# Performance work log

Measured on AMD Instinct MI355X. Metric: run time of the kernel, lower is better.

## Reference

```python
import jax, jax.numpy as jnp
import numpy as np

N = 100000      # nodes on each bipartite side
E = 1600000     # edges
D_IN = 128      # input feature dim
H, C = 2, 50    # heads, per-head out channels
B = 64          # graphs in batch
NEG_SLOPE = 0.2 # GATConv leaky_relu slope


def setup_inputs() -> dict:
    key = jax.random.key(0)
    ks = jax.random.split(key, 12)
    glorot = lambda k, shape: (jax.random.uniform(k, shape, jnp.float32, -1.0, 1.0)
                               * jnp.sqrt(6.0 / (shape[0] + shape[-1])))
    return {
        "x_s": jax.random.normal(ks[0], (N, D_IN), jnp.float32),
        "x_t": jax.random.normal(ks[1], (N, D_IN), jnp.float32),
        "edge_index": jax.random.randint(ks[2], (2, E), 0, N, jnp.int64),
        "distances": jax.random.uniform(ks[3], (E,), jnp.float32),
        "x_s_batch": jnp.sort(jax.random.randint(ks[4], (N,), 0, B, jnp.int64)),
        "x_t_batch": jnp.sort(jax.random.randint(ks[5], (N,), 0, B, jnp.int64)),
        "W_src": glorot(ks[6], (D_IN, H * C)),
        "W_dst": glorot(ks[7], (D_IN, H * C)),
        "att_src": glorot(ks[8], (H, C)),
        "att_dst": glorot(ks[9], (H, C)),
        "bias_conv": jnp.zeros((H * C,), jnp.float32),
        "fc_w": glorot(ks[10], (H * C, 1)),
        "fc_b": jnp.zeros((1,), jnp.float32),
    }


def reference(x_s, x_t, edge_index, distances, x_s_batch, x_t_batch,
              W_src, W_dst, att_src, att_dst, bias_conv, fc_w, fc_b):
    src, dst = edge_index[0], edge_index[1]
    # Bipartite GATConv (edge_attr ignored: built with edge_dim=None)
    hs = (x_s @ W_src).reshape(N, H, C)            # [N,H,C]
    ht = (x_t @ W_dst).reshape(N, H, C)
    a_src = jnp.einsum('nhc,hc->nh', hs, att_src)  # [N,H]
    a_dst = jnp.einsum('nhc,hc->nh', ht, att_dst)
    e = jax.nn.leaky_relu(a_src[src] + a_dst[dst], NEG_SLOPE)   # [E,H]
    # segment softmax over edges sharing a target node
    m = jax.ops.segment_max(e, dst, num_segments=N)             # [N,H]
    ex = jnp.exp(e - m[dst])
    denom = jax.ops.segment_sum(ex, dst, num_segments=N)
    alpha = ex / (denom[dst] + 1e-16)                           # [E,H]
    # scatter-aggregate weighted source messages
    msg = alpha[:, :, None] * hs[src]                           # [E,H,C]
    out = jax.ops.segment_sum(msg, dst, num_segments=N)         # [N,H,C]
    out = out.reshape(N, H * C) + bias_conv
    x = jax.nn.relu(out)
    # global mean pool (original uses x_s_batch)
    pooled = jax.ops.segment_sum(x, x_s_batch, num_segments=B)
    counts = jax.ops.segment_sum(jnp.ones((N,), x.dtype), x_s_batch, num_segments=B)
    pooled = pooled / jnp.maximum(counts, 1.0)[:, None]         # [B,H*C]
    y = pooled @ fc_w + fc_b                                    # [B,1]
    return y.squeeze(-1)
```

## Files before the change

kernel.cpp:

```cpp
#include <hip/hip_runtime.h>
#include <math.h>

#define D_IN 128
#define HC 100
#define PW 128
#define CAP 64
#define NEG 0.2f
#define BINSH 6
#define NBIN 1563
#define BCAP 1408
#define ACH 4096
#define YSLOT 32

typedef __attribute__((ext_vector_type(8))) short short8;
typedef __attribute__((ext_vector_type(4))) float f32x4;
typedef __attribute__((ext_vector_type(2))) float f32x2;

__device__ __forceinline__ float lrelu(float x){ return x > 0.f ? x : NEG*x; }

__device__ __forceinline__ unsigned short f2bf(float f){
  union { float f; unsigned u; } v; v.f = f;
  unsigned r = v.u + 0x7fffu + ((v.u >> 16) & 1u);
  return (unsigned short)(r >> 16);
}
__device__ __forceinline__ float bflo(unsigned u){
  union { unsigned x; float f; } v; v.x = u << 16; return v.f;
}
__device__ __forceinline__ float bfhi(unsigned u){
  union { unsigned x; float f; } v; v.x = u & 0xffff0000u; return v.f;
}

__global__ __launch_bounds__(256) void k_init(const float* __restrict__ Wd,
    const float* __restrict__ attd, const float* __restrict__ Ws,
    const float* __restrict__ bias, const float* __restrict__ fcw,
    const float* __restrict__ fcb, const int* __restrict__ xsb,
    float* __restrict__ wv, float* __restrict__ bias_p, float* __restrict__ fcwp,
    unsigned short* __restrict__ Wp, float* __restrict__ invb,
    int* __restrict__ bincnt, float* __restrict__ ypart,
    float* __restrict__ y, int N, int B){
  __shared__ int lo[257];
  int t = threadIdx.x;
  if (blockIdx.x == 0){
    int h = t >> 7, k = t & 127;
    float s = 0.f;
    #pragma unroll
    for (int c = 0; c < 50; ++c) s += Wd[k*HC + h*50 + c] * attd[h*50 + c];
    wv[t] = s;
    if (t < 128){
      bool cv = (t < 50) || (t >= 56 && t < 106);
      int c = (t < 50) ? t : t - 6;
      bias_p[t] = cv ? bias[c] : 0.f;
      fcwp[t]   = cv ? fcw[c]  : 0.f;
    }
    if (t < B) y[t] = fcb[0];
    for (int i = t; i < NBIN; i += 256) bincnt[i] = 0;
    if (t <= B && t < 257){
      int key = t, l = 0, hi = N;
      while (l < hi){ int mid = (l+hi)>>1; if (xsb[mid] < key) l = mid+1; else hi = mid; }
      lo[t] = l;
    }
    __syncthreads();
    if (t < B){
      int c = lo[t+1] - lo[t];
      invb[t] = 1.f / (float)((c > 0) ? c : 1);
    }
  } else if (blockIdx.x == 1){
    for (int idx = t; idx < 1792; idx += 256){
      int ct = idx >> 8, kk = (idx >> 6) & 3, lane = idx & 63;
      int kb = kk*32 + (lane >> 4)*8;
      int c  = ct*16 + (lane & 15);
      #pragma unroll
      for (int j = 0; j < 8; ++j){
        float v = (c < HC) ? Ws[(size_t)(kb + j)*HC + c] : 0.f;
        Wp[idx*8 + j] = f2bf(v);
      }
    }
  } else {
    float4 z = make_float4(0.f,0.f,0.f,0.f);
    float4* yp4 = (float4*)ypart + (size_t)(blockIdx.x - 2)*8192;
    for (int i = t; i < 8192; i += 256) yp4[i] = z;
  }
}

__global__ __launch_bounds__(256) void k_fused(
    const float* __restrict__ x_s, const unsigned short* __restrict__ Wp,
    const float* __restrict__ atts, unsigned short* __restrict__ hsb,
    float* __restrict__ a_src,
    const float* __restrict__ x_t, const float* __restrict__ wv,
    float* __restrict__ a_dst,
    const int* __restrict__ ei, int* __restrict__ bincnt,
    int2* __restrict__ ebuf,
    int N, int E, int Gg)
{
  __shared__ __align__(16) unsigned char smem[17408];
  int t = threadIdx.x;
  int bid = blockIdx.x;

  if (bid < Gg){
    unsigned short* hls = (unsigned short*)smem;
    float* wsh = (float*)(smem + 16384);
    int lane = t & 63, w = t >> 6;
    int qr = lane & 15, qq = lane >> 4;
    int row0 = bid*64;

    wsh[t] = wv[t];
    for (int i = t; i < 4096; i += 256) ((unsigned*)hls)[i] = 0u;

    int arow = row0 + w*16 + qr;
    bool rv = arow < N;
    short8 afr[4];
    const float* xp = x_s + (size_t)arow*D_IN + qq*8;
    #pragma unroll
    for (int kk = 0; kk < 4; ++kk){
      float4 v0 = make_float4(0.f,0.f,0.f,0.f), v1 = v0;
      if (rv){ v0 = *(const float4*)(xp + kk*32); v1 = *(const float4*)(xp + kk*32 + 4); }
      short8 a;
      a[0]=(short)f2bf(v0.x); a[1]=(short)f2bf(v0.y); a[2]=(short)f2bf(v0.z); a[3]=(short)f2bf(v0.w);
      a[4]=(short)f2bf(v1.x); a[5]=(short)f2bf(v1.y); a[6]=(short)f2bf(v1.z); a[7]=(short)f2bf(v1.w);
      afr[kk] = a;
    }

    __syncthreads();

    float pd0 = 0.f, pd1 = 0.f;
    const float* xtp = x_t + (size_t)arow*D_IN + qq*8;
    #pragma unroll
    for (int kk = 0; kk < 4; ++kk){
      float4 u0 = make_float4(0.f,0.f,0.f,0.f), u1 = u0;
      if (rv){ u0 = *(const float4*)(xtp + kk*32); u1 = *(const float4*)(xtp + kk*32 + 4); }
      int kb = qq*8 + kk*32;
      pd0 += u0.x*wsh[kb+0] + u0.y*wsh[kb+1] + u0.z*wsh[kb+2] + u0.w*wsh[kb+3]
           + u1.x*wsh[kb+4] + u1.y*wsh[kb+5] + u1.z*wsh[kb+6] + u1.w*wsh[kb+7];
      pd1 += u0.x*wsh[128+kb+0] + u0.y*wsh[128+kb+1] + u0.z*wsh[128+kb+2] + u0.w*wsh[128+kb+3]
           + u1.x*wsh[128+kb+4] + u1.y*wsh[128+kb+5] + u1.z*wsh[128+kb+6] + u1.w*wsh[128+kb+7];
    }
    pd0 += __shfl_xor(pd0, 16, 64); pd0 += __shfl_xor(pd0, 32, 64);
    pd1 += __shfl_xor(pd1, 16, 64); pd1 += __shfl_xor(pd1, 32, 64);
    if (qq == 0 && rv){ a_dst[arow*2] = pd0; a_dst[arow*2+1] = pd1; }

    f32x4 acc[7];
    #pragma unroll
    for (int ct = 0; ct < 7; ++ct) acc[ct] = (f32x4){0.f,0.f,0.f,0.f};
    #pragma unroll
    for (int kk = 0; kk < 4; ++kk){
      #pragma unroll
      for (int ct = 0; ct < 7; ++ct){
        short8 b = *(const short8*)&Wp[(size_t)((ct*4+kk)*64 + lane)*8];
        acc[ct] = __builtin_amdgcn_mfma_f32_16x16x32_bf16(afr[kk], b, acc[ct], 0, 0, 0);
      }
    }

    float p0[4] = {0,0,0,0}, p1[4] = {0,0,0,0};
    #pragma unroll
    for (int ct = 0; ct < 7; ++ct){
      int c = ct*16 + qr;
      if (c < HC){
        float av = atts[c];
        #pragma unroll
        for (int r = 0; r < 4; ++r){
          float v = acc[ct][r];
          if (c < 50) p0[r] += v*av; else p1[r] += v*av;
        }
      }
    }
    #pragma unroll
    for (int d = 1; d < 16; d <<= 1){
      #pragma unroll
      for (int r = 0; r < 4; ++r){
        p0[r] += __shfl_xor(p0[r], d, 64);
        p1[r] += __shfl_xor(p1[r], d, 64);
      }
    }
    if (qr == 0){
      #pragma unroll
      for (int r = 0; r < 4; ++r){
        int row = row0 + w*16 + qq*4 + r;
        if (row < N){ a_src[row*2] = p0[r]; a_src[row*2+1] = p1[r]; }
      }
    }

    #pragma unroll
    for (int ct = 0; ct < 7; ++ct){
      int c = ct*16 + qr;
      if (c < HC){
        int p = (c < 50) ? c : c + 6;
        #pragma unroll
        for (int r = 0; r < 4; ++r)
          hls[(w*16 + qq*4 + r)*PW + p] = f2bf(acc[ct][r]);
      }
    }
    __syncthreads();
    unsigned* hg = (unsigned*)(hsb + (size_t)row0*PW);
    for (int i = t; i < 4096; i += 256) hg[i] = ((unsigned*)hls)[i];

  } else {
    int* cnt   = (int*)smem;
    int* gbase = (int*)smem + NBIN;
    int e0 = (bid - Gg) * ACH;
    for (int i = t; i < NBIN; i += 256) cnt[i] = 0;
    __syncthreads();

    int src[16], dst[16], rank[16];
    #pragma unroll
    for (int j = 0; j < 4; ++j){
      int e = e0 + t*16 + j*4;
      bool in = (e + 4 <= E);
      int4 s4 = in ? *(const int4*)&ei[e]     : make_int4(0,0,0,0);
      int4 d4 = in ? *(const int4*)&ei[E + e] : make_int4(-1,-1,-1,-1);
      src[j*4+0]=s4.x; src[j*4+1]=s4.y; src[j*4+2]=s4.z; src[j*4+3]=s4.w;
      dst[j*4+0]=d4.x; dst[j*4+1]=d4.y; dst[j*4+2]=d4.z; dst[j*4+3]=d4.w;
    }
    #pragma unroll
    for (int j = 0; j < 16; ++j)
      rank[j] = (dst[j] >= 0) ? atomicAdd(&cnt[dst[j] >> BINSH], 1) : -1;
    __syncthreads();
    for (int i = t; i < NBIN; i += 256)
      gbase[i] = (cnt[i] > 0) ? atomicAdd(&bincnt[i], cnt[i]) : 0;
    __syncthreads();
    #pragma unroll
    for (int j = 0; j < 16; ++j){
      if (rank[j] >= 0){
        int b = dst[j] >> BINSH;
        int gp = gbase[b] + rank[j];
        if (gp < BCAP) ebuf[(size_t)b*BCAP + gp] = make_int2(src[j], dst[j]);
      }
    }
  }
}

__global__ __launch_bounds__(256) void k_agg(const int* __restrict__ bincnt,
    const int2* __restrict__ ebuf, const float* __restrict__ a_src,
    const float* __restrict__ a_dst, const unsigned short* __restrict__ hsb,
    const float* __restrict__ bias_p, const float* __restrict__ fcwp,
    const int* __restrict__ xsb, float* __restrict__ ypart, int N)
{
  __shared__ int lsrc[64*CAP];
  __shared__ int lcnt[64];
  int t = threadIdx.x, b = blockIdx.x;
  if (t < 64) lcnt[t] = 0;
  __syncthreads();
  int nE = bincnt[b]; if (nE > BCAP) nE = BCAP;
  const int2* eb = ebuf + (size_t)b*BCAP;
  for (int i = t; i < nE; i += 256){
    int2 sd = eb[i];
    int ld = sd.y & 63;
    int p = atomicAdd(&lcnt[ld], 1);
    if (p < CAP) lsrc[ld*CAP + p] = sd.x;
  }
  __syncthreads();

  int lane = t & 63, w = t >> 6;
  int k = lane & 15, g = lane >> 4;
  bool actv = (k < 14);
  bool hsel = (k >= 7);

#define PREF(vv, e) { int s_ = __shfl(sreg, (e), 64); \
    vv = (actv && (e) < deg) ? *(const uint4*)&hsb[(size_t)s_*PW + k*8] \
                             : make_uint4(0u,0u,0u,0u); }

#define CONS(vv, e) { float a0_ = __shfl(al0, (e), 64); float a1_ = __shfl(al1, (e), 64); \
    float a_ = hsel ? a1_ : a0_; f32x2 av_ = {a_, a_}; \
    f32x2 h0_ = {bflo(vv.x), bfhi(vv.x)}; acc0 += av_*h0_; \
    f32x2 h1_ = {bflo(vv.y), bfhi(vv.y)}; acc1 += av_*h1_; \
    f32x2 h2_ = {bflo(vv.z), bfhi(vv.z)}; acc2 += av_*h2_; \
    f32x2 h3_ = {bflo(vv.w), bfhi(vv.w)}; acc3 += av_*h3_; }

  for (int it = 0; it < 16; ++it){
    int nl = w*16 + it;
    int n  = b*64 + nl;
    if (n >= N) break;
    int deg = lcnt[nl]; if (deg > CAP) deg = CAP;
    float2 ad = *(const float2*)&a_dst[n*2];
    int sreg = (lane < deg) ? lsrc[nl*CAP + lane] : 0;

    uint4 v0, v1, v2, v3;
    PREF(v0, g) PREF(v1, 4+g) PREF(v2, 8+g) PREF(v3, 12+g)

    float e0 = -INFINITY, e1 = -INFINITY;
    if (lane < deg){
      float2 as = *(const float2*)&a_src[sreg*2];
      e0 = lrelu(as.x + ad.x);
      e1 = lrelu(as.y + ad.y);
    }
    float m0 = e0, m1 = e1;
    if (deg > 32){ m0 = fmaxf(m0, __shfl_xor(m0,32,64)); m1 = fmaxf(m1, __shfl_xor(m1,32,64)); }
    if (deg > 16){ m0 = fmaxf(m0, __shfl_xor(m0,16,64)); m1 = fmaxf(m1, __shfl_xor(m1,16,64)); }
    #pragma unroll
    for (int d = 8; d >= 1; d >>= 1){
      m0 = fmaxf(m0, __shfl_xor(m0,d,64)); m1 = fmaxf(m1, __shfl_xor(m1,d,64));
    }
    float x0 = 0.f, x1 = 0.f;
    if (lane < deg){ x0 = __expf(e0 - m0); x1 = __expf(e1 - m1); }
    float d0 = x0, d1 = x1;
    if (deg > 32){ d0 += __shfl_xor(d0,32,64); d1 += __shfl_xor(d1,32,64); }
    if (deg > 16){ d0 += __shfl_xor(d0,16,64); d1 += __shfl_xor(d1,16,64); }
    #pragma unroll
    for (int d = 8; d >= 1; d >>= 1){ d0 += __shfl_xor(d0,d,64); d1 += __shfl_xor(d1,d,64); }
    float inv0 = __builtin_amdgcn_rcpf(d0 + 1e-16f);
    float inv1 = __builtin_amdgcn_rcpf(d1 + 1e-16f);
    float al0 = x0 * inv0, al1 = x1 * inv1;

    f32x2 acc0 = {0.f,0.f}, acc1 = {0.f,0.f}, acc2 = {0.f,0.f}, acc3 = {0.f,0.f};
    int base = 0;
    for (;;){
      CONS(v0, base+g);
      if (base + 4 >= deg) break;
      CONS(v1, base+4+g);
      if (base + 8 >= deg) break;
      CONS(v2, base+8+g);
      if (base + 12 >= deg) break;
      CONS(v3, base+12+g);
      base += 16;
      if (base >= deg) break;
      PREF(v0, base+g) PREF(v1, base+4+g) PREF(v2, base+8+g) PREF(v3, base+12+g)
    }

    float acc[8] = {acc0.x, acc0.y, acc1.x, acc1.y, acc2.x, acc2.y, acc3.x, acc3.y};
    #pragma unroll
    for (int j = 0; j < 8; ++j){
      acc[j] += __shfl_xor(acc[j], 16, 64);
      acc[j] += __shfl_xor(acc[j], 32, 64);
    }

    float s = 0.f;
    if (g == 0 && actv){
      float4 b0 = *(const float4*)&bias_p[k*8];
      float4 b1 = *(const float4*)&bias_p[k*8 + 4];
      float4 f0 = *(const float4*)&fcwp[k*8];
      float4 f1 = *(const float4*)&fcwp[k*8 + 4];
      s  = fmaxf(acc[0]+b0.x, 0.f)*f0.x + fmaxf(acc[1]+b0.y, 0.f)*f0.y
         + fmaxf(acc[2]+b0.z, 0.f)*f0.z + fmaxf(acc[3]+b0.w, 0.f)*f0.w
         + fmaxf(acc[4]+b1.x, 0.f)*f1.x + fmaxf(acc[5]+b1.y, 0.f)*f1.y
         + fmaxf(acc[6]+b1.z, 0.f)*f1.z + fmaxf(acc[7]+b1.w, 0.f)*f1.w;
    }
    #pragma unroll
    for (int d = 1; d <= 8; d <<= 1) s += __shfl_xor(s, d, 64);
    if (lane == 0){
      int bb = xsb[n];
      atomicAdd(&ypart[(size_t)((bb*YSLOT + (b & (YSLOT-1))) << 5)], s);
    }
  }
#undef PREF
#undef CONS
}

__global__ __launch_bounds__(64) void k_red(const float* __restrict__ ypart,
    const float* __restrict__ invb, float* __restrict__ y)
{
  int b = blockIdx.x, t = threadIdx.x;
  float v = (t < YSLOT) ? ypart[(size_t)((b*YSLOT + t) << 5)] : 0.f;
  #pragma unroll
  for (int d = 16; d >= 1; d >>= 1) v += __shfl_xor(v, d, 64);
  if (t == 0) y[b] += v * invb[b];
}

extern "C" void kernel_launch(void* const* d_in, const int* in_sizes, int n_in,
                              void* d_out, int out_size, void* d_ws, size_t ws_size,
                              hipStream_t stream)
{
  const float* x_s  = (const float*)d_in[0];
  const float* x_t  = (const float*)d_in[1];
  const int*   ei   = (const int*)d_in[2];
  const int*   xsb  = (const int*)d_in[4];
  const float* Ws   = (const float*)d_in[6];
  const float* Wd   = (const float*)d_in[7];
  const float* atts = (const float*)d_in[8];
  const float* attd = (const float*)d_in[9];
  const float* bias = (const float*)d_in[10];
  const float* fcw  = (const float*)d_in[11];
  const float* fcb  = (const float*)d_in[12];
  float* y = (float*)d_out;

  const int N = in_sizes[4];
  const int E = in_sizes[3];
  const int B = out_size;

  char* p = (char*)d_ws;
  auto carve = [&](size_t bytes)->char*{
    char* r = p; p += (bytes + 255) & ~(size_t)255; return r;
  };
  float*          wv     = (float*)         carve(256*4);
  float*          a_src  = (float*)         carve((size_t)N*2*4);
  float*          a_dst  = (float*)         carve((size_t)N*2*4);
  unsigned short* hsb    = (unsigned short*)carve((size_t)(N+64)*PW*2);
  float*          bias_p = (float*)         carve(128*4);
  float*          fcwp   = (float*)         carve(128*4);
  unsigned short* Wp     = (unsigned short*)carve((size_t)1792*8*2);
  float*          invb   = (float*)         carve(256*4);
  int*            bincnt = (int*)           carve(2048*4);
  float*          ypart  = (float*)         carve((size_t)B*YSLOT*32*4);
  int2*           ebuf   = (int2*)          carve((size_t)NBIN*BCAP*8);

  const int Gg = (N + 63) / 64;
  const int Gb = (E + ACH - 1) / ACH;

  k_init  <<<4, 256, 0, stream>>>(Wd, attd, Ws, bias, fcw, fcb, xsb,
                                  wv, bias_p, fcwp, Wp, invb, bincnt, ypart, y, N, B);
  k_fused <<<Gg + Gb, 256, 0, stream>>>(x_s, Wp, atts, hsb, a_src,
                                        x_t, wv, a_dst,
                                        ei, bincnt, ebuf, N, E, Gg);
  k_agg   <<<NBIN, 256, 0, stream>>>(bincnt, ebuf, a_src, a_dst, hsb,
                                     bias_p, fcwp, xsb, ypart, N);
  k_red   <<<B, 64, 0, stream>>>(ypart, invb, y);
}
```

Before: 297.6 us.

## Pack edge buffer entries to 32-bit and split aggregation bins across two blocks

Edge-bin entries now pack the source index (17 bits) and the local destination slot into one int, halving the edge buffer's write and read traffic. The aggregation kernel runs two 128-thread blocks per bin, each keeping only its half of the destination nodes, which gives more, smaller blocks at the cost of every bin being read twice. The fused kernel now puts the edge-binning blocks first so they are scheduled ahead of the GEMM blocks, and the x_t loads are hoisted before the barrier. The packing assumes N fits in 17 bits.

```diff
diff --git a/kernel.cpp b/kernel.cpp
--- a/kernel.cpp
+++ b/kernel.cpp
@@ -11,6 +11,7 @@
 #define BCAP 1408
 #define ACH 4096
 #define YSLOT 32
+#define SRCM 0x1FFFF
 
 typedef __attribute__((ext_vector_type(8))) short short8;
 typedef __attribute__((ext_vector_type(4))) float f32x4;
@@ -89,19 +90,19 @@
     const float* __restrict__ x_t, const float* __restrict__ wv,
     float* __restrict__ a_dst,
     const int* __restrict__ ei, int* __restrict__ bincnt,
-    int2* __restrict__ ebuf,
-    int N, int E, int Gg)
+    int* __restrict__ ebuf,
+    int N, int E, int Gb)
 {
   __shared__ __align__(16) unsigned char smem[17408];
   int t = threadIdx.x;
   int bid = blockIdx.x;
 
-  if (bid < Gg){
+  if (bid >= Gb){
     unsigned short* hls = (unsigned short*)smem;
     float* wsh = (float*)(smem + 16384);
     int lane = t & 63, w = t >> 6;
     int qr = lane & 15, qq = lane >> 4;
-    int row0 = bid*64;
+    int row0 = (bid - Gb)*64;
 
     wsh[t] = wv[t];
     for (int i = t; i < 4096; i += 256) ((unsigned*)hls)[i] = 0u;
@@ -109,7 +110,8 @@
     int arow = row0 + w*16 + qr;
     bool rv = arow < N;
     short8 afr[4];
-    const float* xp = x_s + (size_t)arow*D_IN + qq*8;
+    const float* xp  = x_s + (size_t)arow*D_IN + qq*8;
+    const float* xtp = x_t + (size_t)arow*D_IN + qq*8;
     #pragma unroll
     for (int kk = 0; kk < 4; ++kk){
       float4 v0 = make_float4(0.f,0.f,0.f,0.f), v1 = v0;
@@ -119,15 +121,19 @@
       a[4]=(short)f2bf(v1.x); a[5]=(short)f2bf(v1.y); a[6]=(short)f2bf(v1.z); a[7]=(short)f2bf(v1.w);
       afr[kk] = a;
     }
+    float4 u[8];
+    #pragma unroll
+    for (int kk = 0; kk < 4; ++kk){
+      u[2*kk]   = rv ? *(const float4*)(xtp + kk*32)     : make_float4(0.f,0.f,0.f,0.f);
+      u[2*kk+1] = rv ? *(const float4*)(xtp + kk*32 + 4) : make_float4(0.f,0.f,0.f,0.f);
+    }
 
     __syncthreads();
 
     float pd0 = 0.f, pd1 = 0.f;
-    const float* xtp = x_t + (size_t)arow*D_IN + qq*8;
     #pragma unroll
     for (int kk = 0; kk < 4; ++kk){
-      float4 u0 = make_float4(0.f,0.f,0.f,0.f), u1 = u0;
-      if (rv){ u0 = *(const float4*)(xtp + kk*32); u1 = *(const float4*)(xtp + kk*32 + 4); }
+      float4 u0 = u[2*kk], u1 = u[2*kk+1];
       int kb = qq*8 + kk*32;
       pd0 += u0.x*wsh[kb+0] + u0.y*wsh[kb+1] + u0.z*wsh[kb+2] + u0.w*wsh[kb+3]
            + u1.x*wsh[kb+4] + u1.y*wsh[kb+5] + u1.z*wsh[kb+6] + u1.w*wsh[kb+7];
@@ -196,7 +202,7 @@
   } else {
     int* cnt   = (int*)smem;
     int* gbase = (int*)smem + NBIN;
-    int e0 = (bid - Gg) * ACH;
+    int e0 = bid * ACH;
     for (int i = t; i < NBIN; i += 256) cnt[i] = 0;
     __syncthreads();
 
@@ -222,30 +228,33 @@
       if (rank[j] >= 0){
         int b = dst[j] >> BINSH;
         int gp = gbase[b] + rank[j];
-        if (gp < BCAP) ebuf[(size_t)b*BCAP + gp] = make_int2(src[j], dst[j]);
+        if (gp < BCAP) ebuf[(size_t)b*BCAP + gp] = src[j] | ((dst[j] & 63) << 17);
       }
     }
   }
 }
 
-__global__ __launch_bounds__(256) void k_agg(const int* __restrict__ bincnt,
-    const int2* __restrict__ ebuf, const float* __restrict__ a_src,
+__global__ __launch_bounds__(128) void k_agg(const int* __restrict__ bincnt,
+    const int* __restrict__ ebuf, const float* __restrict__ a_src,
     const float* __restrict__ a_dst, const unsigned short* __restrict__ hsb,
     const float* __restrict__ bias_p, const float* __restrict__ fcwp,
     const int* __restrict__ xsb, float* __restrict__ ypart, int N)
 {
-  __shared__ int lsrc[64*CAP];
-  __shared__ int lcnt[64];
+  __shared__ int lsrc[32*CAP];
+  __shared__ int lcnt[32];
   int t = threadIdx.x, b = blockIdx.x;
-  if (t < 64) lcnt[t] = 0;
+  int bin = b >> 1, half = b & 1;
+  if (t < 32) lcnt[t] = 0;
   __syncthreads();
-  int nE = bincnt[b]; if (nE > BCAP) nE = BCAP;
-  const int2* eb = ebuf + (size_t)b*BCAP;
-  for (int i = t; i < nE; i += 256){
-    int2 sd = eb[i];
-    int ld = sd.y & 63;
-    int p = atomicAdd(&lcnt[ld], 1);
-    if (p < CAP) lsrc[ld*CAP + p] = sd.x;
+  int nE = bincnt[bin]; if (nE > BCAP) nE = BCAP;
+  const int* eb = ebuf + (size_t)bin*BCAP;
+  for (int i = t; i < nE; i += 128){
+    int e = eb[i];
+    int ld = (e >> 17) & 63;
+    if ((ld >> 5) == half){
+      int p = atomicAdd(&lcnt[ld & 31], 1);
+      if (p < CAP) lsrc[(ld & 31)*CAP + p] = e & SRCM;
+    }
   }
   __syncthreads();
 
@@ -267,7 +276,7 @@
 
   for (int it = 0; it < 16; ++it){
     int nl = w*16 + it;
-    int n  = b*64 + nl;
+    int n  = bin*64 + half*32 + nl;
     if (n >= N) break;
     int deg = lcnt[nl]; if (deg > CAP) deg = CAP;
     float2 ad = *(const float2*)&a_dst[n*2];
@@ -389,17 +398,17 @@
   float*          invb   = (float*)         carve(256*4);
   int*            bincnt = (int*)           carve(2048*4);
   float*          ypart  = (float*)         carve((size_t)B*YSLOT*32*4);
-  int2*           ebuf   = (int2*)          carve((size_t)NBIN*BCAP*8);
+  int*            ebuf   = (int*)           carve((size_t)NBIN*BCAP*4);
 
   const int Gg = (N + 63) / 64;
   const int Gb = (E + ACH - 1) / ACH;
 
   k_init  <<<4, 256, 0, stream>>>(Wd, attd, Ws, bias, fcw, fcb, xsb,
                                   wv, bias_p, fcwp, Wp, invb, bincnt, ypart, y, N, B);
-  k_fused <<<Gg + Gb, 256, 0, stream>>>(x_s, Wp, atts, hsb, a_src,
+  k_fused <<<Gb + Gg, 256, 0, stream>>>(x_s, Wp, atts, hsb, a_src,
                                         x_t, wv, a_dst,
-                                        ei, bincnt, ebuf, N, E, Gg);
-  k_agg   <<<NBIN, 256, 0, stream>>>(bincnt, ebuf, a_src, a_dst, hsb,
-                                     bias_p, fcwp, xsb, ypart, N);
+                                        ei, bincnt, ebuf, N, E, Gb);
+  k_agg   <<<NBIN*2, 128, 0, stream>>>(bincnt, ebuf, a_src, a_dst, hsb,
+                                       bias_p, fcwp, xsb, ypart, N);
   k_red   <<<B, 64, 0, stream>>>(ypart, invb, y);
 }
```

New measurement: 275.9 us. 7.3% less time.
